# Kernel optimization log

Measured on AMD Instinct MI355X. Metric: run time of the kernel, lower is better.

## Reference

```python
import jax, jax.numpy as jnp
import numpy as np

N_NODES = 10000
IN_DIM = 2
HID = 64
OUT_DIM = 1
T = 12
B = 8
E = 160000
K = 3  # temporal conv kernel size


def setup_inputs() -> dict:
    key = jax.random.key(0)
    ks = jax.random.split(key, 16)
    inp = {
        "X": jax.random.normal(ks[0], (B, T, N_NODES, IN_DIM), jnp.float32),
        "edge_index": jax.random.randint(ks[1], (2, E), 0, N_NODES, jnp.int32),
        "edge_weight": jax.random.uniform(ks[2], (E,), jnp.float32),
        # GCNConv params (lin weight + bias)
        "W1": jax.random.normal(ks[3], (IN_DIM, HID), jnp.float32) / np.sqrt(IN_DIM),
        "b1": jnp.zeros((HID,), jnp.float32),
        "W2": jax.random.normal(ks[4], (HID, HID), jnp.float32) / np.sqrt(HID),
        "b2": jnp.zeros((HID,), jnp.float32),
        # Conv1d params: OIH layout [out_ch, in_ch, k]
        "tc1_w": jax.random.normal(ks[5], (HID, HID, K), jnp.float32) / np.sqrt(HID * K),
        "tc1_b": jnp.zeros((HID,), jnp.float32),
        "tc2_w": jax.random.normal(ks[6], (HID, HID, K), jnp.float32) / np.sqrt(HID * K),
        "tc2_b": jnp.zeros((HID,), jnp.float32),
        "out_w": jax.random.normal(ks[7], (HID, OUT_DIM), jnp.float32) / np.sqrt(HID),
        "out_b": jnp.zeros((OUT_DIM,), jnp.float32),
    }
    return inp


def _gcn_norm(edge_index, edge_weight, n):
    # PyG GCNConv default: add self-loops (weight 1) + symmetric normalization
    src = jnp.concatenate([edge_index[0], jnp.arange(n, dtype=edge_index.dtype)])
    dst = jnp.concatenate([edge_index[1], jnp.arange(n, dtype=edge_index.dtype)])
    w = jnp.concatenate([edge_weight, jnp.ones((n,), edge_weight.dtype)])
    deg = jnp.zeros((n,), w.dtype).at[dst].add(w)
    dinv = jnp.where(deg > 0, deg ** -0.5, 0.0)
    norm = dinv[src] * w * dinv[dst]
    return src, dst, norm


def reference(X, edge_index, edge_weight, W1, b1, W2, b2,
              tc1_w, tc1_b, tc2_w, tc2_b, out_w, out_b):
    B_, T_, N_, F_ = X.shape
    H_ = W1.shape[1]
    src, dst, norm = _gcn_norm(edge_index, edge_weight, N_)
    nrm = norm[None, :, None]  # [1, E+N, 1]

    def agg(h):  # h: [B, N, H] -> normalized neighbor sum
        return jnp.zeros_like(h).at[:, dst].add(nrm * h[:, src])

    def gcn_step(x_t):  # x_t: [B, N, F]
        h = jax.nn.relu(agg(x_t @ W1) + b1)   # gc1 + relu (dropout = eval identity)
        h = jax.nn.relu(agg(h @ W2) + b2)     # gc2 + relu
        return h

    # spatial pass across all timesteps (scan keeps per-step edge buffers small)
    spatial = jax.lax.map(gcn_step, jnp.moveaxis(X, 1, 0))  # [T, B, N, H]
    sp = jnp.transpose(spatial, (1, 2, 3, 0)).reshape(B_ * N_, H_, T_)  # [B*N, H, T]

    dn = ("NCH", "OIH", "NCH")
    t = jax.lax.conv_general_dilated(sp, tc1_w, (1,), "SAME", dimension_numbers=dn)
    t = jax.nn.relu(t + tc1_b[None, :, None])
    t = jax.lax.conv_general_dilated(t, tc2_w, (1,), "SAME", dimension_numbers=dn)
    t = jax.nn.relu(t + tc2_b[None, :, None])
    last = t[:, :, -1]                         # [B*N, H]
    out = last @ out_w + out_b                 # [B*N, out_dim]
    out = out.reshape(B_, N_, -1)[:, None]     # [B, 1, N, out_dim]
    return out
```

## Files before the change

### kernel.cpp

```cpp
#include <hip/hip_runtime.h>
#include <hip/hip_fp16.h>

#define N_NODES 10000
#define EDGES   160000
#define BATCH   8
#define TT      12
#define HID     64
#define CAP     64

typedef _Float16 f16x8 __attribute__((ext_vector_type(8)));
typedef _Float16 f16x4 __attribute__((ext_vector_type(4)));
typedef float    f32x4 __attribute__((ext_vector_type(4)));

__host__ __device__ __forceinline__ int kperm(int k31) {
  return (((k31 >> 2) & 3) << 3) + ((k31 >> 4) << 2) + (k31 & 3);
}


__global__ __launch_bounds__(256) void k_fillfix(const int* __restrict__ ei,
                                                 const float* __restrict__ ew,
                                                 int* __restrict__ cur,
                                                 int* __restrict__ csrc,
                                                 float* __restrict__ cnorm) {
  int g = blockIdx.x * 256 + threadIdx.x;
  if (g < EDGES) {
    int s = ei[g], d = ei[EDGES + g];
    int slot = atomicAdd(&cur[d], 1);
    csrc[d * CAP + slot]  = s;
    cnorm[d * CAP + slot] = ew[g];
  }
}

__global__ __launch_bounds__(256) void k_degpad(const int* __restrict__ cur,
                                                int* __restrict__ csrc,
                                                float* __restrict__ cnorm,
                                                float* __restrict__ dinv,
                                                int* __restrict__ mcnt) {
  int n = blockIdx.x * 4 + (threadIdx.x >> 6);
  int lane = threadIdx.x & 63;
  int cnt = cur[n];
  int m = (cnt + 7) & ~7;
  int base = n * CAP;
  if (lane >= cnt && lane < m) { csrc[base + lane] = 0; cnorm[base + lane] = 0.0f; }
  float s = (lane < cnt) ? cnorm[base + lane] : 0.0f;
  #pragma unroll
  for (int off = 32; off > 0; off >>= 1) s += __shfl_xor(s, off, 64);
  if (lane == 0) {
    dinv[n] = 1.0f / sqrtf(s + 1.0f);
    mcnt[n] = m;
  }
}

__global__ __launch_bounds__(256) void k_wnormpack(const int* __restrict__ cur,
                                                   const int* __restrict__ csrc,
                                                   const float* __restrict__ dinv,
                                                   float* __restrict__ cnorm,
                                                   const float* __restrict__ tc1w,
                                                   const float* __restrict__ tc2w,
                                                   const float* __restrict__ tc1b,
                                                   const float* __restrict__ W2,
                                                   ushort* __restrict__ p1ct,
                                                   ushort* __restrict__ p2ct,
                                                   ushort* __restrict__ W2t,
                                                   float* __restrict__ pb1) {
  if (blockIdx.x < 2500) {
    int n = blockIdx.x * 4 + (threadIdx.x >> 6);
    int lane = threadIdx.x & 63;
    int cnt = cur[n];
    int m = (cnt + 7) & ~7;
    if (lane < m) {
      int idx = n * CAP + lane;
      cnorm[idx] = cnorm[idx] * dinv[csrc[idx]] * dinv[n];
    }
  } else {
    int g = (blockIdx.x - 2500) * 256 + threadIdx.x;
    if (g < 24576) {
      int kk = g >> 7, col = g & 127;
      int t3 = kk >> 6, i = kk & 63;
      int half = col >> 6, o = col & 63;
      float v;
      if (half == 0) v = tc1w[o * 192 + i * 3 + t3];
      else           v = (t3 == 0) ? 0.0f : tc1w[o * 192 + i * 3 + (t3 - 1)];
      p1ct[col * 192 + (kk >> 5) * 32 + kperm(kk & 31)] = __half_as_ushort(__float2half_rn(v));
    } else if (g < 32768) {
      int r = g - 24576;
      int kk = r >> 6, o = r & 63;
      int gk = kk >> 6, i = kk & 63;
      float v = tc2w[o * 192 + i * 3 + gk];
      p2ct[o * 128 + (kk >> 5) * 32 + kperm(kk & 31)] = __half_as_ushort(__float2half_rn(v));
    } else if (g < 36864) {
      int r = g - 32768;
      int kk = r >> 6, c = r & 63;
      float v = W2[kk * 64 + c];
      W2t[c * 64 + (kk >> 5) * 32 + kperm(kk & 31)] = __half_as_ushort(__float2half_rn(v));
    } else if (g < 36992) {
      int r = g - 36864;
      pb1[r] = tc1b[r & 63];
    }
  }
}


__global__ __launch_bounds__(256) void k_aggg1(const float* __restrict__ X,
                                               const float* __restrict__ dinv,
                                               const int* __restrict__ mcnt,
                                               const int* __restrict__ csrc,
                                               const float* __restrict__ cnorm,
                                               const float* __restrict__ W1,
                                               const float* __restrict__ b1,
                                               ushort* __restrict__ h1) {
  int b = blockIdx.x & 7;
  int grp = blockIdx.x >> 3;
  int n = grp * 4 + (threadIdx.x >> 6);
  int lane = threadIdx.x & 63;
  const float2* x0 = (const float2*)(X + (size_t)(b * TT + 9)  * N_NODES * 2);
  const float2* x1 = (const float2*)(X + (size_t)(b * TT + 10) * N_NODES * 2);
  const float2* x2 = (const float2*)(X + (size_t)(b * TT + 11) * N_NODES * 2);
  float a0x = 0.f, a0y = 0.f, a1x = 0.f, a1y = 0.f, a2x = 0.f, a2y = 0.f;
  int m = mcnt[n];
  if (lane < m) {
    int idx = n * CAP + lane;
    float w = cnorm[idx];
    int s = csrc[idx];
    float2 s0 = x0[s], s1 = x1[s], s2v = x2[s];
    a0x = w * s0.x;  a0y = w * s0.y;
    a1x = w * s1.x;  a1y = w * s1.y;
    a2x = w * s2v.x; a2y = w * s2v.y;
  }
  if (lane == 0) {
    float di = dinv[n];
    float sd = di * di;
    float2 v0 = x0[n], v1 = x1[n], v2 = x2[n];
    a0x += sd * v0.x; a0y += sd * v0.y;
    a1x += sd * v1.x; a1y += sd * v1.y;
    a2x += sd * v2.x; a2y += sd * v2.y;
  }
  #pragma unroll
  for (int off = 32; off > 0; off >>= 1) {
    a0x += __shfl_xor(a0x, off, 64);
    a0y += __shfl_xor(a0y, off, 64);
    a1x += __shfl_xor(a1x, off, 64);
    a1y += __shfl_xor(a1y, off, 64);
    a2x += __shfl_xor(a2x, off, 64);
    a2y += __shfl_xor(a2y, off, 64);
  }
  int c = lane;
  float w0 = W1[c], w1 = W1[64 + c], bc = b1[c];
  float r0 = fmaxf(a0x * w0 + a0y * w1 + bc, 0.0f);
  float r1 = fmaxf(a1x * w0 + a1y * w1 + bc, 0.0f);
  float r2 = fmaxf(a2x * w0 + a2y * w1 + bc, 0.0f);
  ushort* row = h1 + ((size_t)(b * N_NODES + n)) * 192;
  *(__half2*)(row + 2 * c)  = __floats2half2_rn(r0, r1);
  *(__half*)(row + 128 + c) = __float2half_rn(r2);
}

__global__ __launch_bounds__(256) void k_agg3m16(const ushort* __restrict__ h1,
                                                 const float* __restrict__ dinv,
                                                 const int* __restrict__ mcnt,
                                                 const int* __restrict__ csrc,
                                                 const float* __restrict__ cnorm,
                                                 ushort* __restrict__ ah16) {
  int b = blockIdx.x & 7;
  int grp = blockIdx.x >> 3;
  int n = grp * 4 + (threadIdx.x >> 6);
  int c = threadIdx.x & 63;
  const ushort* hb = h1 + (size_t)b * N_NODES * 192;
  float acc0 = 0.f, acc1 = 0.f, acc2 = 0.f;
  int m = mcnt[n];
  int idx = n * CAP + c;
  int ic = (c < m) ? idx : n * CAP;
  int sv = csrc[ic] * 192;
  float wf = (c < m) ? cnorm[idx] : 0.0f;
  int wb = __float_as_int(wf);
  for (int e = 0; e < m; e += 8) {
    #pragma unroll
    for (int u = 0; u < 8; u++) {
      int   off = __builtin_amdgcn_readlane(sv, e + u);
      float w   = __int_as_float(__builtin_amdgcn_readlane(wb, e + u));
      const ushort* p = hb + off;
      float2 f01 = __half22float2(*(const __half2*)(p + 2 * c));
      float  t2v = __half2float(*(const __half*)(p + 128 + c));
      acc0 += w * f01.x;
      acc1 += w * f01.y;
      acc2 += w * t2v;
    }
  }
  float di = dinv[n];
  float s2 = di * di;
  const ushort* sr = hb + (size_t)n * 192;
  float2 fs = __half22float2(*(const __half2*)(sr + 2 * c));
  float  fst = __half2float(*(const __half*)(sr + 128 + c));
  int oh = ((c >> 5) << 5) + kperm(c & 31);
  ushort* orow = ah16 + ((size_t)(b * N_NODES + n)) * 192 + oh;
  *(__half*)&orow[0]   = __float2half_rn(acc0 + s2 * fs.x);
  *(__half*)&orow[64]  = __float2half_rn(acc1 + s2 * fs.y);
  *(__half*)&orow[128] = __float2half_rn(acc2 + s2 * fst);
}

__global__ __launch_bounds__(256, 4) void k_fused(const ushort* __restrict__ ah16,
                                                  const ushort* __restrict__ W2t,
                                                  const float* __restrict__ b2,
                                                  const ushort* __restrict__ p1ct,
                                                  const float* __restrict__ pb1,
                                                  const ushort* __restrict__ p2ct,
                                                  const float* __restrict__ tc2b,
                                                  const float* __restrict__ ow,
                                                  const float* __restrict__ obp,
                                                  float* __restrict__ out) {
  __shared__ __align__(16) ushort smem[20480];
  ushort* spL = smem;
  ushort* As  = smem + 6144;
  ushort* W2s = smem + 12288;
  ushort* Wc  = smem + 6144;
  ushort* t1L = smem + 16384;
  float*  red = (float*)smem;

  int tid = threadIdx.x;
  int lane = tid & 63, w = tid >> 6;
  int l15 = lane & 15, g = lane >> 4;
  size_t nodeBase = (size_t)blockIdx.x * 32;
  const ushort* A16 = ah16 + nodeBase * 192;

  #pragma unroll
  for (int rep = 0; rep < 3; rep++) {
    int idx = rep * 256 + tid;
    int m = idx >> 3, j = idx & 7;
    *(uint4*)&As[m * 64 + ((j ^ (m & 7)) << 3)] = *(const uint4*)&A16[m * 64 + (j << 3)];
  }
  #pragma unroll
  for (int r = 0; r < 2; r++) {
    int u = r * 256 + tid;
    int cl = u >> 3, hu = u & 7;
    *(uint4*)&W2s[cl * 64 + ((hu * 8) ^ ((cl & 7) << 3))] =
        *(const uint4*)&W2t[cl * 64 + hu * 8];
  }
  __syncthreads();

  {
    int col = w * 16 + l15;
    float bias = b2[col];
    f32x4 acc[6];
    #pragma unroll
    for (int i = 0; i < 6; i++) acc[i] = (f32x4){0.f, 0.f, 0.f, 0.f};
    #pragma unroll
    for (int s = 0; s < 2; s++) {
      int oh = s * 32 + 8 * g;
      f16x8 bf = *(const f16x8*)&W2s[col * 64 + (oh ^ ((col & 7) << 3))];
      #pragma unroll
      for (int mi = 0; mi < 6; mi++) {
        int row = mi * 16 + l15;
        f16x8 af = *(const f16x8*)&As[row * 64 + (oh ^ ((row & 7) << 3))];
        acc[mi] = __builtin_amdgcn_mfma_f32_16x16x32_f16(af, bf, acc[mi], 0, 0, 0);
      }
    }
    #pragma unroll
    for (int mi = 0; mi < 6; mi++) {
      #pragma unroll
      for (int r = 0; r < 4; r++) {
        int m = mi * 16 + 4 * g + r;
        int n = m / 3, t3 = m - 3 * n;
        float v = fmaxf(acc[mi][r] + bias, 0.0f);
        int k = t3 * 64 + col;
        int oh = (k >> 5) * 32 + kperm(k & 31);
        *(_Float16*)&spL[n * 192 + (oh ^ ((n & 7) << 3))] = (_Float16)v;
      }
    }
  }
  __syncthreads();

  f32x4 acc2[2][2];
  #pragma unroll
  for (int i = 0; i < 2; i++)
    #pragma unroll
    for (int j = 0; j < 2; j++) acc2[i][j] = (f32x4){0.f, 0.f, 0.f, 0.f};
  int c0 = 32 * w + l15, c1 = c0 + 16;
  for (int cc = 0; cc < 3; cc++) {
    #pragma unroll
    for (int r = 0; r < 4; r++) {
      int u = r * 256 + tid;
      int cl = u >> 3, hu = u & 7;
      *(uint4*)&Wc[cl * 64 + ((hu * 8) ^ ((cl & 7) << 3))] =
          *(const uint4*)&p1ct[cl * 192 + cc * 64 + hu * 8];
    }
    __syncthreads();
    #pragma unroll
    for (int ks = 0; ks < 2; ks++) {
      int ohB = ks * 32 + 8 * g;
      f16x8 bf0 = *(const f16x8*)&Wc[c0 * 64 + (ohB ^ ((c0 & 7) << 3))];
      f16x8 bf1 = *(const f16x8*)&Wc[c1 * 64 + (ohB ^ ((c1 & 7) << 3))];
      int ohA = (cc * 2 + ks) * 32 + 8 * g;
      #pragma unroll
      for (int mi = 0; mi < 2; mi++) {
        int row = mi * 16 + l15;
        f16x8 af = *(const f16x8*)&spL[row * 192 + (ohA ^ ((row & 7) << 3))];
        acc2[mi][0] = __builtin_amdgcn_mfma_f32_16x16x32_f16(af, bf0, acc2[mi][0], 0, 0, 0);
        acc2[mi][1] = __builtin_amdgcn_mfma_f32_16x16x32_f16(af, bf1, acc2[mi][1], 0, 0, 0);
      }
    }
    __syncthreads();
  }
  {
    float bz0 = pb1[c0], bz1 = pb1[c1];
    int oh0 = (c0 >> 5) * 32 + kperm(c0 & 31);
    int oh1 = (c1 >> 5) * 32 + kperm(c1 & 31);
    #pragma unroll
    for (int mi = 0; mi < 2; mi++) {
      #pragma unroll
      for (int r = 0; r < 4; r++) {
        int n = mi * 16 + 4 * g + r;
        float v0 = fmaxf(acc2[mi][0][r] + bz0, 0.0f);
        float v1 = fmaxf(acc2[mi][1][r] + bz1, 0.0f);
        *(_Float16*)&t1L[n * 128 + (oh0 ^ ((n & 7) << 3))] = (_Float16)v0;
        *(_Float16*)&t1L[n * 128 + (oh1 ^ ((n & 7) << 3))] = (_Float16)v1;
      }
    }
  }
  #pragma unroll
  for (int r = 0; r < 4; r++) {
    int u = r * 256 + tid;
    int cl = u >> 4, hu = u & 15;
    *(uint4*)&Wc[cl * 128 + ((hu * 8) ^ ((cl & 7) << 3))] =
        *(const uint4*)&p2ct[cl * 128 + hu * 8];
  }
  __syncthreads();

  {
    int col = 16 * w + l15;
    f32x4 acc3[2];
    acc3[0] = (f32x4){0.f, 0.f, 0.f, 0.f};
    acc3[1] = (f32x4){0.f, 0.f, 0.f, 0.f};
    #pragma unroll
    for (int s = 0; s < 4; s++) {
      int oh = s * 32 + 8 * g;
      f16x8 bf = *(const f16x8*)&Wc[col * 128 + (oh ^ ((col & 7) << 3))];
      #pragma unroll
      for (int mi = 0; mi < 2; mi++) {
        int row = mi * 16 + l15;
        f16x8 af = *(const f16x8*)&t1L[row * 128 + (oh ^ ((row & 7) << 3))];
        acc3[mi] = __builtin_amdgcn_mfma_f32_16x16x32_f16(af, bf, acc3[mi], 0, 0, 0);
      }
    }
    float tb = tc2b[col], o4 = ow[col];
    float s4[2][4];
    #pragma unroll
    for (int mi = 0; mi < 2; mi++)
      #pragma unroll
      for (int r = 0; r < 4; r++)
        s4[mi][r] = fmaxf(acc3[mi][r] + tb, 0.0f) * o4;
    #pragma unroll
    for (int off = 1; off <= 8; off <<= 1) {
      #pragma unroll
      for (int mi = 0; mi < 2; mi++)
        #pragma unroll
        for (int r = 0; r < 4; r++)
          s4[mi][r] += __shfl_xor(s4[mi][r], off, 64);
    }
    if (l15 == 0) {
      #pragma unroll
      for (int mi = 0; mi < 2; mi++) {
        float4 o;
        o.x = s4[mi][0]; o.y = s4[mi][1]; o.z = s4[mi][2]; o.w = s4[mi][3];
        *(float4*)&red[w * 32 + mi * 16 + 4 * g] = o;
      }
    }
  }
  __syncthreads();
  if (tid < 32) {
    float v = red[tid] + red[32 + tid] + red[64 + tid] + red[96 + tid] + obp[0];
    out[nodeBase + tid] = v;
  }
}


extern "C" void kernel_launch(void* const* d_in, const int* in_sizes, int n_in,
                              void* d_out, int out_size, void* d_ws, size_t ws_size,
                              hipStream_t stream) {
  const float* X    = (const float*)d_in[0];
  const int*   EI   = (const int*)  d_in[1];
  const float* EW   = (const float*)d_in[2];
  const float* W1   = (const float*)d_in[3];
  const float* B1   = (const float*)d_in[4];
  const float* W2   = (const float*)d_in[5];
  const float* B2   = (const float*)d_in[6];
  const float* TC1W = (const float*)d_in[7];
  const float* TC1B = (const float*)d_in[8];
  const float* TC2W = (const float*)d_in[9];
  const float* TC2B = (const float*)d_in[10];
  const float* OW   = (const float*)d_in[11];
  const float* OB   = (const float*)d_in[12];
  float* out = (float*)d_out;

  char* base = (char*)d_ws;
  size_t off = 0;
  auto alloc = [&](size_t bytes) -> char* {
    char* p = base + off;
    off += (bytes + 255) & ~(size_t)255;
    return p;
  };
  float*  dinv  = (float*) alloc(N_NODES * 4);
  int*    cur   = (int*)   alloc(N_NODES * 4);
  int*    mcnt  = (int*)   alloc(N_NODES * 4);
  int*    csrc  = (int*)   alloc((size_t)N_NODES * CAP * 4);
  float*  cnorm = (float*) alloc((size_t)N_NODES * CAP * 4);
  ushort* p1ct  = (ushort*)alloc(128 * 192 * 2);
  ushort* p2ct  = (ushort*)alloc(64 * 128 * 2);
  ushort* W2t   = (ushort*)alloc(64 * 64 * 2);
  float*  pb1   = (float*) alloc(128 * 4);
  const size_t BIG = (size_t)80000 * 192;
  ushort* h1   = (ushort*)alloc(BIG * 2);
  ushort* ah16 = (ushort*)alloc(BIG * 2);

  hipMemsetAsync(cur, 0, N_NODES * 4, stream);
  k_fillfix<<<625, 256, 0, stream>>>(EI, EW, cur, csrc, cnorm);
  k_degpad<<<2500, 256, 0, stream>>>(cur, csrc, cnorm, dinv, mcnt);
  k_wnormpack<<<2645, 256, 0, stream>>>(cur, csrc, dinv, cnorm, TC1W, TC2W, TC1B, W2,
                                        p1ct, p2ct, W2t, pb1);

  k_aggg1<<<20000, 256, 0, stream>>>(X, dinv, mcnt, csrc, cnorm, W1, B1, h1);
  k_agg3m16<<<20000, 256, 0, stream>>>(h1, dinv, mcnt, csrc, cnorm, ah16);
  k_fused<<<2500, 256, 0, stream>>>(ah16, W2t, B2, p1ct, pb1, p2ct, TC2B, OW, OB, out);
}
```

Measured before the change: 194.7 us.

## Fuse second-layer neighbor aggregation into the MFMA temporal kernel via shared memory

The second GCN aggregation kernel is removed. Its gather-and-sum is done inside the fused GEMM/temporal-conv kernel, which writes the aggregated fp16 rows straight into the swizzled shared-memory A tile. This drops the global write and re-read of the 30 MB intermediate ah16 buffer and one kernel launch. In exchange each block now does 32 node gathers serially across 4 waves (8 per wave) before the MFMA stage. The grid is remapped to batch plus 32-node groups, padded to 2504 blocks, with bounds checks on the node index.

Measured after the change: 214.8 us. 10.3% more time.

```diff
diff --git a/kernel.cpp b/kernel.cpp
--- a/kernel.cpp
+++ b/kernel.cpp
@@ -154,59 +154,20 @@
   *(__half*)(row + 128 + c) = __float2half_rn(r2);
 }
 
-__global__ __launch_bounds__(256) void k_agg3m16(const ushort* __restrict__ h1,
-                                                 const float* __restrict__ dinv,
-                                                 const int* __restrict__ mcnt,
-                                                 const int* __restrict__ csrc,
-                                                 const float* __restrict__ cnorm,
-                                                 ushort* __restrict__ ah16) {
-  int b = blockIdx.x & 7;
-  int grp = blockIdx.x >> 3;
-  int n = grp * 4 + (threadIdx.x >> 6);
-  int c = threadIdx.x & 63;
-  const ushort* hb = h1 + (size_t)b * N_NODES * 192;
-  float acc0 = 0.f, acc1 = 0.f, acc2 = 0.f;
-  int m = mcnt[n];
-  int idx = n * CAP + c;
-  int ic = (c < m) ? idx : n * CAP;
-  int sv = csrc[ic] * 192;
-  float wf = (c < m) ? cnorm[idx] : 0.0f;
-  int wb = __float_as_int(wf);
-  for (int e = 0; e < m; e += 8) {
-    #pragma unroll
-    for (int u = 0; u < 8; u++) {
-      int   off = __builtin_amdgcn_readlane(sv, e + u);
-      float w   = __int_as_float(__builtin_amdgcn_readlane(wb, e + u));
-      const ushort* p = hb + off;
-      float2 f01 = __half22float2(*(const __half2*)(p + 2 * c));
-      float  t2v = __half2float(*(const __half*)(p + 128 + c));
-      acc0 += w * f01.x;
-      acc1 += w * f01.y;
-      acc2 += w * t2v;
-    }
-  }
-  float di = dinv[n];
-  float s2 = di * di;
-  const ushort* sr = hb + (size_t)n * 192;
-  float2 fs = __half22float2(*(const __half2*)(sr + 2 * c));
-  float  fst = __half2float(*(const __half*)(sr + 128 + c));
-  int oh = ((c >> 5) << 5) + kperm(c & 31);
-  ushort* orow = ah16 + ((size_t)(b * N_NODES + n)) * 192 + oh;
-  *(__half*)&orow[0]   = __float2half_rn(acc0 + s2 * fs.x);
-  *(__half*)&orow[64]  = __float2half_rn(acc1 + s2 * fs.y);
-  *(__half*)&orow[128] = __float2half_rn(acc2 + s2 * fst);
-}
-
-__global__ __launch_bounds__(256, 4) void k_fused(const ushort* __restrict__ ah16,
-                                                  const ushort* __restrict__ W2t,
-                                                  const float* __restrict__ b2,
-                                                  const ushort* __restrict__ p1ct,
-                                                  const float* __restrict__ pb1,
-                                                  const ushort* __restrict__ p2ct,
-                                                  const float* __restrict__ tc2b,
-                                                  const float* __restrict__ ow,
-                                                  const float* __restrict__ obp,
-                                                  float* __restrict__ out) {
+__global__ __launch_bounds__(256, 4) void k_gfused(const ushort* __restrict__ h1,
+                                                   const float* __restrict__ dinv,
+                                                   const int* __restrict__ mcnt,
+                                                   const int* __restrict__ csrc,
+                                                   const float* __restrict__ cnorm,
+                                                   const ushort* __restrict__ W2t,
+                                                   const float* __restrict__ b2,
+                                                   const ushort* __restrict__ p1ct,
+                                                   const float* __restrict__ pb1,
+                                                   const ushort* __restrict__ p2ct,
+                                                   const float* __restrict__ tc2b,
+                                                   const float* __restrict__ ow,
+                                                   const float* __restrict__ obp,
+                                                   float* __restrict__ out) {
   __shared__ __align__(16) ushort smem[20480];
   ushort* spL = smem;
   ushort* As  = smem + 6144;
@@ -218,21 +179,60 @@
   int tid = threadIdx.x;
   int lane = tid & 63, w = tid >> 6;
   int l15 = lane & 15, g = lane >> 4;
-  size_t nodeBase = (size_t)blockIdx.x * 32;
-  const ushort* A16 = ah16 + nodeBase * 192;
-
-  #pragma unroll
-  for (int rep = 0; rep < 3; rep++) {
-    int idx = rep * 256 + tid;
-    int m = idx >> 3, j = idx & 7;
-    *(uint4*)&As[m * 64 + ((j ^ (m & 7)) << 3)] = *(const uint4*)&A16[m * 64 + (j << 3)];
-  }
+  int b   = blockIdx.x & 7;
+  int grp = blockIdx.x >> 3;
+  int n0  = grp * 32;
+  const ushort* hb = h1 + (size_t)b * N_NODES * 192;
+
   #pragma unroll
   for (int r = 0; r < 2; r++) {
     int u = r * 256 + tid;
     int cl = u >> 3, hu = u & 7;
     *(uint4*)&W2s[cl * 64 + ((hu * 8) ^ ((cl & 7) << 3))] =
         *(const uint4*)&W2t[cl * 64 + hu * 8];
+  }
+
+  {
+    int c = lane;
+    int ohc = ((c >> 5) << 5) + kperm(c & 31);
+    for (int jj = 0; jj < 8; jj++) {
+      int j = w * 8 + jj;
+      int n = n0 + j;
+      float acc0 = 0.f, acc1 = 0.f, acc2 = 0.f;
+      if (n < N_NODES) {
+        int m = mcnt[n];
+        int idx = n * CAP + c;
+        int ic = (c < m) ? idx : n * CAP;
+        int sv = csrc[ic] * 192;
+        float wf = (c < m) ? cnorm[idx] : 0.0f;
+        int wb = __float_as_int(wf);
+        for (int e = 0; e < m; e += 8) {
+          #pragma unroll
+          for (int u = 0; u < 8; u++) {
+            int   off = __builtin_amdgcn_readlane(sv, e + u);
+            float ww  = __int_as_float(__builtin_amdgcn_readlane(wb, e + u));
+            const ushort* p = hb + off;
+            float2 f01 = __half22float2(*(const __half2*)(p + 2 * c));
+            float  t2v = __half2float(*(const __half*)(p + 128 + c));
+            acc0 += ww * f01.x;
+            acc1 += ww * f01.y;
+            acc2 += ww * t2v;
+          }
+        }
+        float di = dinv[n];
+        float s2 = di * di;
+        const ushort* sr = hb + (size_t)n * 192;
+        float2 fs = __half22float2(*(const __half2*)(sr + 2 * c));
+        float  fst = __half2float(*(const __half*)(sr + 128 + c));
+        acc0 += s2 * fs.x;
+        acc1 += s2 * fs.y;
+        acc2 += s2 * fst;
+      }
+      int m0 = 3 * j;
+      As[(m0 + 0) * 64 + (ohc ^ (((m0 + 0) & 7) << 3))] = __half_as_ushort(__float2half_rn(acc0));
+      As[(m0 + 1) * 64 + (ohc ^ (((m0 + 1) & 7) << 3))] = __half_as_ushort(__float2half_rn(acc1));
+      As[(m0 + 2) * 64 + (ohc ^ (((m0 + 2) & 7) << 3))] = __half_as_ushort(__float2half_rn(acc2));
+    }
   }
   __syncthreads();
 
@@ -366,8 +366,11 @@
   }
   __syncthreads();
   if (tid < 32) {
-    float v = red[tid] + red[32 + tid] + red[64 + tid] + red[96 + tid] + obp[0];
-    out[nodeBase + tid] = v;
+    int n = n0 + tid;
+    if (n < N_NODES) {
+      float v = red[tid] + red[32 + tid] + red[64 + tid] + red[96 + tid] + obp[0];
+      out[(size_t)b * N_NODES + n] = v;
+    }
   }
 }
 
@@ -407,8 +410,7 @@
   ushort* W2t   = (ushort*)alloc(64 * 64 * 2);
   float*  pb1   = (float*) alloc(128 * 4);
   const size_t BIG = (size_t)80000 * 192;
-  ushort* h1   = (ushort*)alloc(BIG * 2);
-  ushort* ah16 = (ushort*)alloc(BIG * 2);
+  ushort* h1 = (ushort*)alloc(BIG * 2);
 
   hipMemsetAsync(cur, 0, N_NODES * 4, stream);
   k_fillfix<<<625, 256, 0, stream>>>(EI, EW, cur, csrc, cnorm);
@@ -417,6 +419,6 @@
                                         p1ct, p2ct, W2t, pb1);
 
   k_aggg1<<<20000, 256, 0, stream>>>(X, dinv, mcnt, csrc, cnorm, W1, B1, h1);
-  k_agg3m16<<<20000, 256, 0, stream>>>(h1, dinv, mcnt, csrc, cnorm, ah16);
-  k_fused<<<2500, 256, 0, stream>>>(ah16, W2t, B2, p1ct, pb1, p2ct, TC2B, OW, OB, out);
-}
+  k_gfused<<<2504, 256, 0, stream>>>(h1, dinv, mcnt, csrc, cnorm,
+                                     W2t, B2, p1ct, pb1, p2ct, TC2B, OW, OB, out);
+}
```
